# Performance work log

Measured on AMD Instinct MI355X. Metric: run time of the kernel, lower is better.

## Reference

```python
import jax, jax.numpy as jnp
import numpy as np


def _sage_mean_layer(x, src, dst, W_self, W_neigh, b):
    # DGL SAGEConv('mean'): h_neigh = mean_{u in N(v)} x_u ; out = x@W_self + h_neigh@W_neigh + b
    n = x.shape[0]
    msg_sum = jax.ops.segment_sum(x[src], dst, num_segments=n)          # [N, D] scatter-add
    deg = jax.ops.segment_sum(jnp.ones_like(dst, dtype=x.dtype), dst, num_segments=n)
    h_neigh = msg_sum / jnp.maximum(deg, 1.0)[:, None]                   # zero-degree nodes -> 0
    return x @ W_self + h_neigh @ W_neigh + b


def setup_inputs() -> dict:
    key = jax.random.key(0)
    ks = jax.random.split(key, 9)
    N, E, D_in, D_hid, D_out = 50000, 800000, 128, 128, 128
    s = lambda d: 1.0 / np.sqrt(d)
    return {
        "x": jax.random.normal(ks[0], (N, D_in), dtype=jnp.float32),
        "src": jax.random.randint(ks[1], (E,), 0, N, dtype=jnp.int32),
        "dst": jax.random.randint(ks[2], (E,), 0, N, dtype=jnp.int32),
        "W1_self": jax.random.uniform(ks[3], (D_in, D_hid), jnp.float32, -s(D_in), s(D_in)),
        "W1_neigh": jax.random.uniform(ks[4], (D_in, D_hid), jnp.float32, -s(D_in), s(D_in)),
        "b1": jnp.zeros((D_hid,), jnp.float32),
        "W2_self": jax.random.uniform(ks[5], (D_hid, D_out), jnp.float32, -s(D_hid), s(D_hid)),
        "W2_neigh": jax.random.uniform(ks[6], (D_hid, D_out), jnp.float32, -s(D_hid), s(D_hid)),
        "b2": jnp.zeros((D_out,), jnp.float32),
    }


def reference(x, src, dst, W1_self, W1_neigh, b1, W2_self, W2_neigh, b2):
    # layer 1: SAGEConv -> ELU (dropout is identity in eval mode)
    h = jax.nn.elu(_sage_mean_layer(x, src, dst, W1_self, W1_neigh, b1))
    # layer 2: is_out_layer=True -> no activation
    return _sage_mean_layer(h, src, dst, W2_self, W2_neigh, b2)
```

## Files before the change

### kernel.cpp

```cpp
#include <hip/hip_runtime.h>
#include <hip/hip_bf16.h>
#include <math.h>

#define DD 128
#define CAP 64
#define NSHARD 8

typedef __attribute__((ext_vector_type(8))) short short8;
typedef __attribute__((ext_vector_type(4))) float floatx4;
typedef __attribute__((ext_vector_type(8))) unsigned short ushortx8;


__global__ __launch_bounds__(256) void fill_bucket_shard_kernel(
        const int* __restrict__ src, const int* __restrict__ dst,
        int* __restrict__ cnt, ushort* __restrict__ slot16,
        int E, int shard_size, int stride) {
    int shard = blockIdx.x & (NSHARD - 1);
    int chunk = blockIdx.x >> 3;
    int lo = shard * shard_size;
    int hi = lo + shard_size;
    for (int e = chunk * 256 + threadIdx.x; e < E; e += 4 * stride) {
        int e1 = e + stride, e2 = e + 2 * stride, e3 = e + 3 * stride;
        int d0 = dst[e];
        int d1 = e1 < E ? dst[e1] : -1;
        int d2 = e2 < E ? dst[e2] : -1;
        int d3 = e3 < E ? dst[e3] : -1;
        bool v0 = d0 >= lo && d0 < hi;
        bool v1 = d1 >= lo && d1 < hi;
        bool v2 = d2 >= lo && d2 < hi;
        bool v3 = d3 >= lo && d3 < hi;
        int p0 = 0, p1 = 0, p2 = 0, p3 = 0;
        if (v0) p0 = atomicAdd(&cnt[d0], 1);
        if (v1) p1 = atomicAdd(&cnt[d1], 1);
        if (v2) p2 = atomicAdd(&cnt[d2], 1);
        if (v3) p3 = atomicAdd(&cnt[d3], 1);
        if (v0 && p0 < CAP) slot16[(size_t)d0 * CAP + p0] = (ushort)src[e];
        if (v1 && p1 < CAP) slot16[(size_t)d1 * CAP + p1] = (ushort)src[e1];
        if (v2 && p2 < CAP) slot16[(size_t)d2 * CAP + p2] = (ushort)src[e2];
        if (v3 && p3 < CAP) slot16[(size_t)d3 * CAP + p3] = (ushort)src[e3];
    }
}


__global__ void cast_blocked_kernel(const float* __restrict__ x, ushort* __restrict__ Xc, int n) {
    int i = blockIdx.x * blockDim.x + threadIdx.x;
    if (i >= n * 32) return;
    int node = i >> 5;
    int col = (i & 31) * 4;
    float4 v = *(const float4*)&x[(size_t)node * DD + col];
    __hip_bfloat16 b0 = __float2bfloat16(v.x), b1 = __float2bfloat16(v.y);
    __hip_bfloat16 b2 = __float2bfloat16(v.z), b3 = __float2bfloat16(v.w);
    ushort4 o;
    o.x = *(ushort*)&b0; o.y = *(ushort*)&b1; o.z = *(ushort*)&b2; o.w = *(ushort*)&b3;
    size_t ns = (size_t)n * 32;
    *(ushort4*)&Xc[(size_t)(col >> 5) * ns + (size_t)node * 32 + (col & 31)] = o;
}

__global__ void pack_w_kernel(const float* __restrict__ W1a, const float* __restrict__ W1b,
                              const float* __restrict__ W2a, const float* __restrict__ W2b,
                              ushort* __restrict__ Wp1, ushort* __restrict__ Wp2) {
    int gid = blockIdx.x * blockDim.x + threadIdx.x;
    int layer = gid >> 15;
    int r = gid & 32767;
    int j = r & 7;
    int lane = (r >> 3) & 63;
    int nt = (r >> 9) & 7;
    int ks = r >> 12;
    int k = ks * 32 + (lane >> 4) * 8 + j;
    int col = nt * 16 + (lane & 15);
    const float* W = layer ? (k < 128 ? W2a : W2b) : (k < 128 ? W1a : W1b);
    float v = W[(k & 127) * DD + col];
    __hip_bfloat16 b = __float2bfloat16(v);
    (layer ? Wp2 : Wp1)[r] = *(ushort*)&b;
}

#define BF2F(u) __uint_as_float((unsigned)(u) << 16)

__global__ __launch_bounds__(256) void agg_mean_kernel(
        const ushort* __restrict__ Xc, const int* __restrict__ cnt,
        const ushort* __restrict__ slot16, ushort* __restrict__ Hnc, int n) {
    int pass = blockIdx.x & 3;
    int lane = threadIdx.x & 63;
    int g = lane >> 2;
    int q = lane & 3;
    int v = (blockIdx.x >> 2) * 64 + (threadIdx.x >> 6) * 16 + g;
    if (v >= n) return;
    size_t ns = (size_t)n * 32;
    const ushort* Xp = Xc + (size_t)pass * ns;
    int d = cnt[v];
    if (d > CAP) d = CAP;

    float acc[8];
#pragma unroll
    for (int j = 0; j < 8; ++j) acc[j] = 0.f;

    const ushort* srow = slot16 + (size_t)v * CAP;
    int i = 0;
    for (; i + 2 <= d; i += 2) {
        int u0 = (int)srow[i];
        int u1 = (int)srow[i + 1];
        ushortx8 y0 = *(const ushortx8*)&Xp[(size_t)u0 * 32 + q * 8];
        ushortx8 y1 = *(const ushortx8*)&Xp[(size_t)u1 * 32 + q * 8];
#pragma unroll
        for (int j = 0; j < 8; ++j)
            acc[j] += BF2F((ushort)y0[j]) + BF2F((ushort)y1[j]);
    }
    if (i < d) {
        int u = (int)srow[i];
        ushortx8 y = *(const ushortx8*)&Xp[(size_t)u * 32 + q * 8];
#pragma unroll
        for (int j = 0; j < 8; ++j) acc[j] += BF2F((ushort)y[j]);
    }

    float inv = 1.0f / (float)(d > 0 ? d : 1);
    ushort tmp[8];
#pragma unroll
    for (int j = 0; j < 8; ++j) {
        __hip_bfloat16 b = __float2bfloat16(acc[j] * inv);
        tmp[j] = *(ushort*)&b;
    }
    uint4 ov;
    ov.x = (unsigned)tmp[0] | ((unsigned)tmp[1] << 16);
    ov.y = (unsigned)tmp[2] | ((unsigned)tmp[3] << 16);
    ov.z = (unsigned)tmp[4] | ((unsigned)tmp[5] << 16);
    ov.w = (unsigned)tmp[6] | ((unsigned)tmp[7] << 16);
    *(uint4*)&Hnc[(size_t)pass * ns + (size_t)v * 32 + q * 8] = ov;
}

__global__ __launch_bounds__(256) void gemm_fused_kernel(
        const ushort* __restrict__ Xc, const ushort* __restrict__ Hnc,
        const ushort* __restrict__ Wp, const float* __restrict__ bias,
        ushort* __restrict__ out_bf16c, float* __restrict__ out_f32,
        int n, int nstrips, int do_elu) {
    int strip = blockIdx.x * 4 + (threadIdx.x >> 6);
    if (strip >= nstrips) return;
    int lane = threadIdx.x & 63;
    int m = lane & 15;
    int quad = lane >> 4;
    size_t ns = (size_t)n * 32;
    const size_t row0 = (size_t)strip * 16;

    floatx4 acc[8];
#pragma unroll
    for (int t = 0; t < 8; ++t) acc[t] = (floatx4){0.f, 0.f, 0.f, 0.f};

#pragma unroll
    for (int ks = 0; ks < 8; ++ks) {
        const ushort* ap = (ks < 4 ? Xc + (size_t)ks * ns : Hnc + (size_t)(ks - 4) * ns)
                           + (row0 + m) * 32 + quad * 8;
        short8 a = *(const short8*)ap;
        const ushort* wp = Wp + ((size_t)(ks * 8) * 64 + lane) * 8;
#pragma unroll
        for (int nt = 0; nt < 8; ++nt) {
            short8 b = *(const short8*)(wp + (size_t)nt * 64 * 8);
            acc[nt] = __builtin_amdgcn_mfma_f32_16x16x32_bf16(a, b, acc[nt], 0, 0, 0);
        }
    }

#pragma unroll
    for (int nt = 0; nt < 8; ++nt) {
        int col = nt * 16 + m;
        float bv = bias[col];
#pragma unroll
        for (int r = 0; r < 4; ++r) {
            size_t row = row0 + quad * 4 + r;
            float v = acc[nt][r] + bv;
            if (do_elu) v = v > 0.f ? v : expm1f(v);
            if (out_f32) {
                out_f32[row * DD + col] = v;
            } else {
                __hip_bfloat16 b = __float2bfloat16(v);
                out_bf16c[(size_t)(nt >> 1) * ns + row * 32 + (nt & 1) * 16 + m] = *(ushort*)&b;
            }
        }
    }
}


extern "C" void kernel_launch(void* const* d_in, const int* in_sizes, int n_in,
                              void* d_out, int out_size, void* d_ws, size_t ws_size,
                              hipStream_t stream) {
    const float* x   = (const float*)d_in[0];
    const int*   src = (const int*)d_in[1];
    const int*   dst = (const int*)d_in[2];
    const float* W1s = (const float*)d_in[3];
    const float* W1n = (const float*)d_in[4];
    const float* b1  = (const float*)d_in[5];
    const float* W2s = (const float*)d_in[6];
    const float* W2n = (const float*)d_in[7];
    const float* b2  = (const float*)d_in[8];
    float* out = (float*)d_out;

    const int N = in_sizes[0] / DD;
    const int E = in_sizes[1];

    char* ws = (char*)d_ws;
    int*    cnt    = (int*)ws;    ws += (size_t)N * 4;
    ushort* slot16 = (ushort*)ws; ws += (size_t)N * CAP * 2;
    ushort* Wp1    = (ushort*)ws; ws += 65536;
    ushort* Wp2    = (ushort*)ws; ws += 65536;
    ushort* Xc     = (ushort*)ws; ws += (size_t)N * DD * 2;
    ushort* Hnc    = (ushort*)ws; ws += (size_t)N * DD * 2;
    ushort* H1c    = (ushort*)ws; ws += (size_t)N * DD * 2;

    (void)hipMemsetAsync(cnt, 0, (size_t)N * 4, stream);
    const int shard_size = (N + NSHARD - 1) / NSHARD;
    const int nchunks = 256;
    fill_bucket_shard_kernel<<<nchunks * NSHARD, 256, 0, stream>>>(
        src, dst, cnt, slot16, E, shard_size, nchunks * 256);

    cast_blocked_kernel<<<(N * 32 + 255) / 256, 256, 0, stream>>>(x, Xc, N);
    pack_w_kernel<<<256, 256, 0, stream>>>(W1s, W1n, W2s, W2n, Wp1, Wp2);

    const int nstrips = N / 16;
    const int gb = (nstrips + 3) / 4;
    const int ab = 4 * ((N + 63) / 64);

    agg_mean_kernel<<<ab, 256, 0, stream>>>(Xc, cnt, slot16, Hnc, N);
    gemm_fused_kernel<<<gb, 256, 0, stream>>>(Xc, Hnc, Wp1, b1, H1c, nullptr, N, nstrips, 1);

    agg_mean_kernel<<<ab, 256, 0, stream>>>(H1c, cnt, slot16, Hnc, N);
    gemm_fused_kernel<<<gb, 256, 0, stream>>>(H1c, Hnc, Wp2, b2, nullptr, out, N, nstrips, 0);
}
```

Before: 246.5 us.

## Merge bucket fill, feature cast and weight pack into one prologue kernel

Replaces three separate prologue launches with one kernel whose block ranges do edge bucketing, x-to-bf16 casting and weight packing. The edge bucketing also drops the 8-way destination sharding, so each thread reads four consecutive edges with int4 loads and atomics land on random nodes instead of shard-local ranges. This removes two launches and the repeated 8x scan of dst, at the cost of less locality in the atomic counter and slot writes. The three roles can now run concurrently on the GPU.

```diff
diff --git a/kernel.cpp b/kernel.cpp
--- a/kernel.cpp
+++ b/kernel.cpp
@@ -4,62 +4,57 @@
 
 #define DD 128
 #define CAP 64
-#define NSHARD 8
 
 typedef __attribute__((ext_vector_type(8))) short short8;
 typedef __attribute__((ext_vector_type(4))) float floatx4;
 typedef __attribute__((ext_vector_type(8))) unsigned short ushortx8;
 
-
-__global__ __launch_bounds__(256) void fill_bucket_shard_kernel(
+__global__ __launch_bounds__(256) void prologue_kernel(
         const int* __restrict__ src, const int* __restrict__ dst,
-        int* __restrict__ cnt, ushort* __restrict__ slot16,
-        int E, int shard_size, int stride) {
-    int shard = blockIdx.x & (NSHARD - 1);
-    int chunk = blockIdx.x >> 3;
-    int lo = shard * shard_size;
-    int hi = lo + shard_size;
-    for (int e = chunk * 256 + threadIdx.x; e < E; e += 4 * stride) {
-        int e1 = e + stride, e2 = e + 2 * stride, e3 = e + 3 * stride;
-        int d0 = dst[e];
-        int d1 = e1 < E ? dst[e1] : -1;
-        int d2 = e2 < E ? dst[e2] : -1;
-        int d3 = e3 < E ? dst[e3] : -1;
-        bool v0 = d0 >= lo && d0 < hi;
-        bool v1 = d1 >= lo && d1 < hi;
-        bool v2 = d2 >= lo && d2 < hi;
-        bool v3 = d3 >= lo && d3 < hi;
-        int p0 = 0, p1 = 0, p2 = 0, p3 = 0;
-        if (v0) p0 = atomicAdd(&cnt[d0], 1);
-        if (v1) p1 = atomicAdd(&cnt[d1], 1);
-        if (v2) p2 = atomicAdd(&cnt[d2], 1);
-        if (v3) p3 = atomicAdd(&cnt[d3], 1);
-        if (v0 && p0 < CAP) slot16[(size_t)d0 * CAP + p0] = (ushort)src[e];
-        if (v1 && p1 < CAP) slot16[(size_t)d1 * CAP + p1] = (ushort)src[e1];
-        if (v2 && p2 < CAP) slot16[(size_t)d2 * CAP + p2] = (ushort)src[e2];
-        if (v3 && p3 < CAP) slot16[(size_t)d3 * CAP + p3] = (ushort)src[e3];
-    }
-}
-
-
-__global__ void cast_blocked_kernel(const float* __restrict__ x, ushort* __restrict__ Xc, int n) {
-    int i = blockIdx.x * blockDim.x + threadIdx.x;
-    if (i >= n * 32) return;
-    int node = i >> 5;
-    int col = (i & 31) * 4;
-    float4 v = *(const float4*)&x[(size_t)node * DD + col];
-    __hip_bfloat16 b0 = __float2bfloat16(v.x), b1 = __float2bfloat16(v.y);
-    __hip_bfloat16 b2 = __float2bfloat16(v.z), b3 = __float2bfloat16(v.w);
-    ushort4 o;
-    o.x = *(ushort*)&b0; o.y = *(ushort*)&b1; o.z = *(ushort*)&b2; o.w = *(ushort*)&b3;
-    size_t ns = (size_t)n * 32;
-    *(ushort4*)&Xc[(size_t)(col >> 5) * ns + (size_t)node * 32 + (col & 31)] = o;
-}
-
-__global__ void pack_w_kernel(const float* __restrict__ W1a, const float* __restrict__ W1b,
-                              const float* __restrict__ W2a, const float* __restrict__ W2b,
-                              ushort* __restrict__ Wp1, ushort* __restrict__ Wp2) {
-    int gid = blockIdx.x * blockDim.x + threadIdx.x;
+        int* __restrict__ cnt, ushort* __restrict__ slot16, int E,
+        const float* __restrict__ x, ushort* __restrict__ Xc, int n,
+        const float* __restrict__ W1a, const float* __restrict__ W1b,
+        const float* __restrict__ W2a, const float* __restrict__ W2b,
+        ushort* __restrict__ Wp1, ushort* __restrict__ Wp2,
+        int fb, int cb) {
+    int b = blockIdx.x;
+    if (b < fb) {
+        int base = (b * 256 + threadIdx.x) * 4;
+        if (base + 3 < E) {
+            int4 d4 = *(const int4*)&dst[base];
+            int4 s4 = *(const int4*)&src[base];
+            int p0 = atomicAdd(&cnt[d4.x], 1);
+            int p1 = atomicAdd(&cnt[d4.y], 1);
+            int p2 = atomicAdd(&cnt[d4.z], 1);
+            int p3 = atomicAdd(&cnt[d4.w], 1);
+            if (p0 < CAP) slot16[(size_t)d4.x * CAP + p0] = (ushort)s4.x;
+            if (p1 < CAP) slot16[(size_t)d4.y * CAP + p1] = (ushort)s4.y;
+            if (p2 < CAP) slot16[(size_t)d4.z * CAP + p2] = (ushort)s4.z;
+            if (p3 < CAP) slot16[(size_t)d4.w * CAP + p3] = (ushort)s4.w;
+        } else {
+            for (int e = base; e < E; ++e) {
+                int d = dst[e];
+                int p = atomicAdd(&cnt[d], 1);
+                if (p < CAP) slot16[(size_t)d * CAP + p] = (ushort)src[e];
+            }
+        }
+        return;
+    }
+    if (b < fb + cb) {
+        int i = (b - fb) * 256 + threadIdx.x;
+        if (i >= n * 32) return;
+        int node = i >> 5;
+        int col = (i & 31) * 4;
+        float4 v = *(const float4*)&x[(size_t)node * DD + col];
+        __hip_bfloat16 b0 = __float2bfloat16(v.x), b1 = __float2bfloat16(v.y);
+        __hip_bfloat16 b2 = __float2bfloat16(v.z), b3 = __float2bfloat16(v.w);
+        ushort4 o;
+        o.x = *(ushort*)&b0; o.y = *(ushort*)&b1; o.z = *(ushort*)&b2; o.w = *(ushort*)&b3;
+        size_t ns = (size_t)n * 32;
+        *(ushort4*)&Xc[(size_t)(col >> 5) * ns + (size_t)node * 32 + (col & 31)] = o;
+        return;
+    }
+    int gid = (b - fb - cb) * 256 + threadIdx.x;
     int layer = gid >> 15;
     int r = gid & 32767;
     int j = r & 7;
@@ -70,8 +65,8 @@
     int col = nt * 16 + (lane & 15);
     const float* W = layer ? (k < 128 ? W2a : W2b) : (k < 128 ? W1a : W1b);
     float v = W[(k & 127) * DD + col];
-    __hip_bfloat16 b = __float2bfloat16(v);
-    (layer ? Wp2 : Wp1)[r] = *(ushort*)&b;
+    __hip_bfloat16 bb = __float2bfloat16(v);
+    (layer ? Wp2 : Wp1)[r] = *(ushort*)&bb;
 }
 
 #define BF2F(u) __uint_as_float((unsigned)(u) << 16)
@@ -204,13 +199,11 @@
     ushort* H1c    = (ushort*)ws; ws += (size_t)N * DD * 2;
 
     (void)hipMemsetAsync(cnt, 0, (size_t)N * 4, stream);
-    const int shard_size = (N + NSHARD - 1) / NSHARD;
-    const int nchunks = 256;
-    fill_bucket_shard_kernel<<<nchunks * NSHARD, 256, 0, stream>>>(
-        src, dst, cnt, slot16, E, shard_size, nchunks * 256);
-
-    cast_blocked_kernel<<<(N * 32 + 255) / 256, 256, 0, stream>>>(x, Xc, N);
-    pack_w_kernel<<<256, 256, 0, stream>>>(W1s, W1n, W2s, W2n, Wp1, Wp2);
+    const int fb = (E / 4 + 255) / 256;
+    const int cb = (N * 32 + 255) / 256;
+    const int pb = 256;
+    prologue_kernel<<<fb + cb + pb, 256, 0, stream>>>(
+        src, dst, cnt, slot16, E, x, Xc, N, W1s, W1n, W2s, W2n, Wp1, Wp2, fb, cb);
 
     const int nstrips = N / 16;
     const int gb = (nstrips + 3) / 4;
```

Result: no change. 246.0 us (-0.2%).
